# Kernel optimization log

Measured on AMD Instinct MI355X. Metric: run time of the kernel, lower is better.

The kernel has to match this reference:

```python
import jax, jax.numpy as jnp
import numpy as np

N_POI = 1_000_000
R = 10_000
D = 128
H = 4
E = 80_000


def setup_inputs() -> dict:
    key = jax.random.key(0)
    ks = jax.random.split(key, 16)
    s = 0.05
    lin = lambda k: jax.random.normal(k, (D, D), jnp.float32) * s
    return {
        "x": jax.random.normal(ks[0], (N_POI, D), jnp.float32),
        "zone": jax.random.randint(ks[1], (N_POI,), 0, R),
        "edge_index": jax.random.randint(ks[2], (2, E), 0, R),
        "num_regions": R,
        "S": jax.random.normal(ks[3], (D,), jnp.float32) * s,  # PMA seed (num_seeds=1)
        "Wq": lin(ks[4]), "bq": jnp.zeros((D,), jnp.float32),
        "Wk": lin(ks[5]), "bk": jnp.zeros((D,), jnp.float32),
        "Wv": lin(ks[6]), "bv": jnp.zeros((D,), jnp.float32),
        "Wo": lin(ks[7]), "bo": jnp.zeros((D,), jnp.float32),
        "Wg": lin(ks[8]), "bg": jnp.zeros((D,), jnp.float32),  # GCNConv weight/bias
        "prelu_w": jnp.full((D,), 0.25, jnp.float32),
    }


def reference(x, zone, edge_index, num_regions, S, Wq, bq, Wk, bk, Wv, bv, Wo, bo, Wg, bg, prelu_w):
    d = x.shape[1]
    dh = d // H
    # --- PMA over each region (segment attention; seed query shared across regions) ---
    q = (S @ Wq + bq).reshape(H, dh)                     # [H, dh]
    k = (x @ Wk + bk).reshape(-1, H, dh)                 # [N, H, dh]
    v = (x @ Wv + bv).reshape(-1, H, dh)                 # [N, H, dh]
    scores = jnp.einsum('nhd,hd->nh', k, q) / jnp.sqrt(jnp.float32(d))  # Set-Transformer scales by sqrt(dim_V)
    smax = jax.ops.segment_max(scores, zone, num_segments=num_regions)  # [R, H]
    smax = jnp.where(jnp.isfinite(smax), smax, 0.0)
    p = jnp.exp(scores - smax[zone])                     # [N, H]
    denom = jax.ops.segment_sum(p, zone, num_segments=num_regions)      # [R, H]
    wv = jax.ops.segment_sum(p[:, :, None] * v, zone, num_segments=num_regions)  # [R, H, dh]
    attn = wv / jnp.maximum(denom, 1e-9)[:, :, None]
    O = (q[None, :, :] + attn).reshape(num_regions, d)   # residual: Q_ + A @ V_
    O = O + jax.nn.relu(O @ Wo + bo)                     # O + relu(fc_o(O))
    # --- GCNConv (symmetric norm, self loops) ---
    row, col = edge_index[0], edge_index[1]
    sl = jnp.arange(num_regions, dtype=row.dtype)
    row = jnp.concatenate([row, sl])
    col = jnp.concatenate([col, sl])
    deg = jax.ops.segment_sum(jnp.ones_like(col, jnp.float32), col, num_segments=num_regions)
    dinv = jnp.where(deg > 0, 1.0 / jnp.sqrt(deg), 0.0)
    norm = dinv[row] * dinv[col]                         # [E + R]
    h = O @ Wg                                           # [R, D]
    agg = jax.ops.segment_sum(norm[:, None] * h[row], col, num_segments=num_regions)
    out = agg + bg
    # --- PReLU ---
    return jnp.where(out >= 0, out, prelu_w[None, :] * out)
```

## Files before the change

### kernel.cpp

```cpp
#include <hip/hip_runtime.h>
#include <math.h>

__global__ __launch_bounds__(256) void k_init(
    int* __restrict__ izero, int n4, int zb,
    const float* __restrict__ S, const float* __restrict__ Wq, const float* __restrict__ bq,
    const float* __restrict__ Wk, const float* __restrict__ bk,
    float* __restrict__ qvec, float* __restrict__ A, float* __restrict__ cvec) {
  if (blockIdx.x < (unsigned)zb) {
    int i = blockIdx.x * blockDim.x + threadIdx.x;
    if (i < n4) reinterpret_cast<int4*>(izero)[i] = make_int4(0, 0, 0, 0);
    return;
  }
  __shared__ float s_S[128];
  __shared__ float s_q[128];
  const int j = threadIdx.x;
  if (j < 128) s_S[j] = S[j];
  __syncthreads();
  if (j < 128) {
    float acc = bq[j];
    for (int i = 0; i < 128; ++i) acc += s_S[i] * Wq[i * 128 + j];
    qvec[j] = acc;
    s_q[j] = acc;
  }
  __syncthreads();
  if (j < 128) {
    const float scale = 0.088388347648318447f;
    for (int h = 0; h < 4; ++h) {
      float a = 0.f;
      for (int d = 0; d < 32; ++d) a += Wk[j * 128 + h * 32 + d] * s_q[h * 32 + d];
      A[j * 4 + h] = a * scale;
    }
    if (j < 4) {
      float cc = 0.f;
      for (int d = 0; d < 32; ++d) cc += bk[j * 32 + d] * s_q[j * 32 + d];
      cvec[j] = cc * scale;
    }
  }
}

__global__ __launch_bounds__(256) void k_hist2(const int* __restrict__ zone, int N,
                                               const int* __restrict__ ecol, int E,
                                               int* __restrict__ counts, int* __restrict__ ecounts) {
  int i = blockIdx.x * blockDim.x + threadIdx.x;
  if (i < N) {
    atomicAdd(&counts[zone[i]], 1);
  } else if (i < N + E) {
    atomicAdd(&ecounts[ecol[i - N]], 1);
  }
}

__global__ __launch_bounds__(256) void k_scan2(const int* __restrict__ counts, const int* __restrict__ ecounts,
                                               int R, int* __restrict__ startb, int* __restrict__ estartb,
                                               float* __restrict__ dinv) {
  __shared__ int part[256];
  const int t = threadIdx.x;
  const bool edges = (blockIdx.x == 1);
  const int* __restrict__ cnt = edges ? ecounts : counts;
  int* __restrict__ outp = edges ? estartb : startb;
  int chunk = (R + 255) / 256;
  int b = t * chunk, e = min(b + chunk, R);
  int s = 0;
  for (int i = b; i < e; ++i) s += cnt[i];
  part[t] = s;
  __syncthreads();
  for (int off = 1; off < 256; off <<= 1) {
    int v = (t >= off) ? part[t - off] : 0;
    __syncthreads();
    part[t] += v;
    __syncthreads();
  }
  int run = part[t] - s;
  for (int i = b; i < e; ++i) {
    outp[i] = run;
    int c = cnt[i];
    run += c;
    if (edges) dinv[i] = rsqrtf((float)(c + 1));
  }
  if (t == 255) outp[R] = part[255];
}

__global__ __launch_bounds__(256) void k_scatter2(
    const int* __restrict__ zone, int N,
    const int* __restrict__ erow, const int* __restrict__ ecol, int E,
    const int* __restrict__ startb, int* __restrict__ cursor, int* __restrict__ perm,
    const int* __restrict__ estartb, int* __restrict__ ecursor, int* __restrict__ erow_s) {
  int i = blockIdx.x * blockDim.x + threadIdx.x;
  if (i < N) {
    int r = zone[i];
    perm[startb[r] + atomicAdd(&cursor[r], 1)] = i;
  } else if (i < N + E) {
    int e = i - N;
    int c = ecol[e];
    erow_s[estartb[c] + atomicAdd(&ecursor[c], 1)] = erow[e];
  }
}

__global__ __launch_bounds__(256) void k_fused(
    const float* __restrict__ x, const int* __restrict__ perm, const int* __restrict__ startb,
    const float* __restrict__ Aw, const float* __restrict__ cvec,
    float* __restrict__ Xagg, float* __restrict__ denom, int R) {
  const int tid = threadIdx.x;
  const int lane = tid & 63;
  const int half = lane >> 5;
  const int sl = lane & 31;
  const int d0 = sl * 4;
  const int myh = lane & 3;
  const int gw = blockIdx.x * 4 + (tid >> 6);
  const int nw = gridDim.x * 4;

  float a[4][4];
#pragma unroll
  for (int dd = 0; dd < 4; ++dd)
#pragma unroll
    for (int h = 0; h < 4; ++h) a[dd][h] = Aw[(d0 + dd) * 4 + h];
  const float cl = cvec[myh];

  for (int r = gw; r < R; r += nw) {
    const int s0 = startb[r], s1 = startb[r + 1];
    float xagg[4][4] = {};
    float dsum[4] = {};

    int base = s0 + half * 8;
    int idx[8];
#pragma unroll
    for (int k = 0; k < 8; ++k) {
      const int j = base + k;
      idx[k] = (j < s1) ? perm[j] : -1;
    }
    for (; base < s1; base += 16) {
      float4 xv[8];
#pragma unroll
      for (int k = 0; k < 8; ++k) {
        xv[k] = (idx[k] >= 0)
              ? *reinterpret_cast<const float4*>(x + (size_t)idx[k] * 128 + d0)
              : make_float4(0.f, 0.f, 0.f, 0.f);
      }
      int idxn[8];
      const int nb = base + 16;
#pragma unroll
      for (int k = 0; k < 8; ++k) {
        const int j = nb + k;
        idxn[k] = (j < s1) ? perm[j] : -1;
      }
      float red[8];
#pragma unroll
      for (int k = 0; k < 8; ++k) {
        const float4 v = xv[k];
        const float p0 = v.x * a[0][0] + v.y * a[1][0] + v.z * a[2][0] + v.w * a[3][0];
        const float p1 = v.x * a[0][1] + v.y * a[1][1] + v.z * a[2][1] + v.w * a[3][1];
        const float p2 = v.x * a[0][2] + v.y * a[1][2] + v.z * a[2][2] + v.w * a[3][2];
        const float p3 = v.x * a[0][3] + v.y * a[1][3] + v.z * a[2][3] + v.w * a[3][3];
        float a01 = (lane & 1) ? p1 : p0;
        float b01 = (lane & 1) ? p0 : p1;
        a01 += __shfl_xor(b01, 1, 64);
        float a23 = (lane & 1) ? p3 : p2;
        float b23 = (lane & 1) ? p2 : p3;
        a23 += __shfl_xor(b23, 1, 64);
        float aa = (lane & 2) ? a23 : a01;
        float bb = (lane & 2) ? a01 : a23;
        aa += __shfl_xor(bb, 2, 64);
        aa += __shfl_xor(aa, 4, 64);
        aa += __shfl_xor(aa, 8, 64);
        aa += __shfl_xor(aa, 16, 64);
        red[k] = aa;
      }
#pragma unroll
      for (int k = 0; k < 8; ++k) {
        const float e0 = (idx[k] >= 0) ? __expf(red[k] + cl) : 0.f;
        const float e1 = __shfl_xor(e0, 1, 64);
        const float e2 = __shfl_xor(e0, 2, 64);
        const float e3 = __shfl_xor(e0, 3, 64);
        dsum[0] += e0; dsum[1] += e1; dsum[2] += e2; dsum[3] += e3;
        const float4 v = xv[k];
        xagg[0][0] += e0 * v.x; xagg[0][1] += e1 * v.x; xagg[0][2] += e2 * v.x; xagg[0][3] += e3 * v.x;
        xagg[1][0] += e0 * v.y; xagg[1][1] += e1 * v.y; xagg[1][2] += e2 * v.y; xagg[1][3] += e3 * v.y;
        xagg[2][0] += e0 * v.z; xagg[2][1] += e1 * v.z; xagg[2][2] += e2 * v.z; xagg[2][3] += e3 * v.z;
        xagg[3][0] += e0 * v.w; xagg[3][1] += e1 * v.w; xagg[3][2] += e2 * v.w; xagg[3][3] += e3 * v.w;
      }
#pragma unroll
      for (int k = 0; k < 8; ++k) idx[k] = idxn[k];
    }

#pragma unroll
    for (int dd = 0; dd < 4; ++dd)
#pragma unroll
      for (int h = 0; h < 4; ++h) xagg[dd][h] += __shfl_xor(xagg[dd][h], 32, 64);
#pragma unroll
    for (int h = 0; h < 4; ++h) dsum[h] += __shfl_xor(dsum[h], 32, 64);

    if (half == 0) {
      const bool m1 = (myh & 1) != 0;
      const bool m2 = (myh & 2) != 0;
      float outv[4][4];
#pragma unroll
      for (int dd = 0; dd < 4; ++dd) {
        const float b0 = m1 ? xagg[dd][1] : xagg[dd][0];
        const float b1 = m1 ? xagg[dd][0] : xagg[dd][1];
        const float b2 = m1 ? xagg[dd][3] : xagg[dd][2];
        const float b3 = m1 ? xagg[dd][2] : xagg[dd][3];
        outv[0][dd] = m2 ? b2 : b0;
        outv[1][dd] = m2 ? b3 : b1;
        outv[2][dd] = m2 ? b0 : b2;
        outv[3][dd] = m2 ? b1 : b3;
      }
#pragma unroll
      for (int h = 0; h < 4; ++h) {
        const float4 v = make_float4(outv[h][0], outv[h][1], outv[h][2], outv[h][3]);
        *reinterpret_cast<float4*>(Xagg + (size_t)r * 512 + h * 128 + d0) = v;
      }
      if (sl == 0) {
        *reinterpret_cast<float4*>(denom + (size_t)r * 4) =
            make_float4(dsum[0], dsum[1], dsum[2], dsum[3]);
      }
    }
  }
}

__global__ __launch_bounds__(256) void k_epilogue(
    const float* __restrict__ Xagg, const float* __restrict__ denom, const float* __restrict__ qvec,
    const float* __restrict__ Wv, const float* __restrict__ bv,
    const float* __restrict__ Wo, const float* __restrict__ bo,
    const float* __restrict__ Wg, float* __restrict__ hout, int R) {
  const int r0 = blockIdx.x * 8;
  const int tid = threadIdx.x;
  __shared__ float s_xa[8 * 512];
  __shared__ float s_den[8 * 4];
  __shared__ float s_O[8 * 128];
  __shared__ float s_O2[8 * 128];

  for (int t = tid; t < 8 * 512; t += 256) {
    int rl = t >> 9;
    s_xa[t] = (r0 + rl < R) ? Xagg[(size_t)r0 * 512 + t] : 0.f;
  }
  if (tid < 32) {
    int rl = tid >> 2;
    s_den[tid] = (r0 + rl < R) ? denom[r0 * 4 + tid] : 1.f;
  }
  __syncthreads();

  for (int o = tid; o < 1024; o += 256) {
    int rl = o >> 7, t = o & 127, h = t >> 5;
    float acc = 0.f;
    const float* xa = &s_xa[rl * 512 + h * 128];
    for (int j = 0; j < 128; j += 4) {
      float4 x4 = *reinterpret_cast<const float4*>(xa + j);
      acc += x4.x * Wv[j * 128 + t] + x4.y * Wv[(j + 1) * 128 + t]
           + x4.z * Wv[(j + 2) * 128 + t] + x4.w * Wv[(j + 3) * 128 + t];
    }
    float dn = s_den[rl * 4 + h];
    float attn = (acc + dn * bv[t]) / fmaxf(dn, 1e-9f);
    s_O[o] = qvec[t] + attn;
  }
  __syncthreads();

  for (int o = tid; o < 1024; o += 256) {
    int rl = o >> 7, t = o & 127;
    float acc = bo[t];
    const float* ov = &s_O[rl * 128];
    for (int j = 0; j < 128; j += 4) {
      float4 x4 = *reinterpret_cast<const float4*>(ov + j);
      acc += x4.x * Wo[j * 128 + t] + x4.y * Wo[(j + 1) * 128 + t]
           + x4.z * Wo[(j + 2) * 128 + t] + x4.w * Wo[(j + 3) * 128 + t];
    }
    s_O2[o] = s_O[o] + fmaxf(acc, 0.f);
  }
  __syncthreads();

  for (int o = tid; o < 1024; o += 256) {
    int rl = o >> 7, t = o & 127;
    float acc = 0.f;
    const float* ov = &s_O2[rl * 128];
    for (int j = 0; j < 128; j += 4) {
      float4 x4 = *reinterpret_cast<const float4*>(ov + j);
      acc += x4.x * Wg[j * 128 + t] + x4.y * Wg[(j + 1) * 128 + t]
           + x4.z * Wg[(j + 2) * 128 + t] + x4.w * Wg[(j + 3) * 128 + t];
    }
    if (r0 + rl < R) hout[(size_t)(r0 + rl) * 128 + t] = acc;
  }
}

__global__ __launch_bounds__(256) void k_gcn(
    const int* __restrict__ estartb, const int* __restrict__ erow_s,
    const float* __restrict__ dinv, const float* __restrict__ hbuf,
    const float* __restrict__ bg, const float* __restrict__ pw,
    float* __restrict__ out, int R) {
  const int r = blockIdx.x * 4 + (threadIdx.x >> 6);
  if (r >= R) return;
  const int lane = threadIdx.x & 63;
  const int d0 = lane * 2;
  const float dr = dinv[r];
  const float2 hc = *reinterpret_cast<const float2*>(hbuf + (size_t)r * 128 + d0);
  float accx = dr * dr * hc.x;
  float accy = dr * dr * hc.y;
  const int e0 = estartb[r], e1 = estartb[r + 1];
  for (int e = e0; e < e1; ++e) {
    const int rr = erow_s[e];
    const float w = dinv[rr] * dr;
    const float2 hv = *reinterpret_cast<const float2*>(hbuf + (size_t)rr * 128 + d0);
    accx += w * hv.x;
    accy += w * hv.y;
  }
  const float2 b = *reinterpret_cast<const float2*>(bg + d0);
  const float2 pv = *reinterpret_cast<const float2*>(pw + d0);
  const float t0 = accx + b.x;
  const float t1 = accy + b.y;
  out[(size_t)r * 128 + d0]     = (t0 >= 0.f) ? t0 : pv.x * t0;
  out[(size_t)r * 128 + d0 + 1] = (t1 >= 0.f) ? t1 : pv.y * t1;
}

extern "C" void kernel_launch(void* const* d_in, const int* in_sizes, int n_in,
                              void* d_out, int out_size, void* d_ws, size_t ws_size,
                              hipStream_t stream) {
  const float* x   = (const float*)d_in[0];
  const int*   zone = (const int*)d_in[1];
  const int*   eidx = (const int*)d_in[2];
  const float* S   = (const float*)d_in[4];
  const float* Wq  = (const float*)d_in[5];
  const float* bq  = (const float*)d_in[6];
  const float* Wk  = (const float*)d_in[7];
  const float* bk  = (const float*)d_in[8];
  const float* Wv  = (const float*)d_in[9];
  const float* bv  = (const float*)d_in[10];
  const float* Wo  = (const float*)d_in[11];
  const float* bo  = (const float*)d_in[12];
  const float* Wg  = (const float*)d_in[13];
  const float* bg  = (const float*)d_in[14];
  const float* pw  = (const float*)d_in[15];
  float* out = (float*)d_out;

  const int N = in_sizes[0] / 128;
  const int E = in_sizes[2] / 2;
  const int R = out_size / 128;
  const int* erow = eidx;
  const int* ecol = eidx + E;

  char* wsb = (char*)d_ws;
  size_t off = 0;
  auto alloc = [&](size_t bytes) -> void* {
    void* p = wsb + off;
    off = (off + bytes + 255) & ~(size_t)255;
    return p;
  };
  int* izero  = (int*)alloc((size_t)4 * R * 4);
  int* counts = izero;
  int* cursor = izero + R;
  int* ecounts= izero + 2 * R;
  int* ecursor= izero + 3 * R;

  float* qvec  = (float*)alloc(128 * 4);
  float* A     = (float*)alloc(512 * 4);
  float* cvec  = (float*)alloc(4 * 4);
  int*   startb = (int*)alloc((size_t)(R + 1) * 4);
  int*   estartb= (int*)alloc((size_t)(R + 1) * 4);
  float* dinv  = (float*)alloc((size_t)R * 4);
  int*   erow_s= (int*)alloc((size_t)E * 4);
  int*   perm  = (int*)alloc((size_t)N * 4);
  float* Xagg  = (float*)alloc((size_t)R * 512 * 4);
  float* denom = (float*)alloc((size_t)R * 4 * 4);
  float* hbuf  = (float*)alloc((size_t)R * 128 * 4);

  const int n4 = R;
  const int zb = (n4 + 255) / 256;
  k_init<<<zb + 1, 256, 0, stream>>>(izero, n4, zb, S, Wq, bq, Wk, bk, qvec, A, cvec);
  k_hist2<<<(N + E + 255) / 256, 256, 0, stream>>>(zone, N, ecol, E, counts, ecounts);
  k_scan2<<<2, 256, 0, stream>>>(counts, ecounts, R, startb, estartb, dinv);
  k_scatter2<<<(N + E + 255) / 256, 256, 0, stream>>>(zone, N, erow, ecol, E,
                                                      startb, cursor, perm, estartb, ecursor, erow_s);
  k_fused<<<1024, 256, 0, stream>>>(x, perm, startb, A, cvec, Xagg, denom, R);
  k_epilogue<<<(R + 7) / 8, 256, 0, stream>>>(Xagg, denom, qvec, Wv, bv, Wo, bo, Wg, hbuf, R);
  k_gcn<<<(R + 3) / 4, 256, 0, stream>>>(estartb, erow_s, dinv, hbuf, bg, pw, out, R);
}
```

Measured before the change: 371.4 us.

## Record atomic slot positions in histogram and dynamically schedule regions per wave

The histogram pass now stores each element's atomic slot index, so the scatter pass no longer repeats atomics on a second cursor array and only reads the stored position. The q/A precompute moves from the zeroing kernel into a third block of the scan kernel. The fused attention kernel replaces its static grid-stride region assignment with a global atomic work counter, so each wave fetches its next region dynamically to balance uneven region sizes. In exchange this adds 4 MB of position buffers to write and read, plus one atomic per region.

```diff
diff --git a/kernel.cpp b/kernel.cpp
--- a/kernel.cpp
+++ b/kernel.cpp
@@ -1,59 +1,59 @@
 #include <hip/hip_runtime.h>
 #include <math.h>
 
-__global__ __launch_bounds__(256) void k_init(
-    int* __restrict__ izero, int n4, int zb,
+__global__ __launch_bounds__(256) void k_zero(int* __restrict__ p, int n4) {
+  int i = blockIdx.x * blockDim.x + threadIdx.x;
+  if (i < n4) reinterpret_cast<int4*>(p)[i] = make_int4(0, 0, 0, 0);
+}
+
+__global__ __launch_bounds__(256) void k_hist2(const int* __restrict__ zone, int N,
+                                               const int* __restrict__ ecol, int E,
+                                               int* __restrict__ counts, int* __restrict__ ecounts,
+                                               int* __restrict__ pos, int* __restrict__ epos) {
+  int i = blockIdx.x * blockDim.x + threadIdx.x;
+  if (i < N) {
+    pos[i] = atomicAdd(&counts[zone[i]], 1);
+  } else if (i < N + E) {
+    int e = i - N;
+    epos[e] = atomicAdd(&ecounts[ecol[e]], 1);
+  }
+}
+
+__global__ __launch_bounds__(256) void k_scan3(
+    const int* __restrict__ counts, const int* __restrict__ ecounts,
+    int R, int* __restrict__ startb, int* __restrict__ estartb, float* __restrict__ dinv,
     const float* __restrict__ S, const float* __restrict__ Wq, const float* __restrict__ bq,
     const float* __restrict__ Wk, const float* __restrict__ bk,
     float* __restrict__ qvec, float* __restrict__ A, float* __restrict__ cvec) {
-  if (blockIdx.x < (unsigned)zb) {
-    int i = blockIdx.x * blockDim.x + threadIdx.x;
-    if (i < n4) reinterpret_cast<int4*>(izero)[i] = make_int4(0, 0, 0, 0);
+  const int t = threadIdx.x;
+  if (blockIdx.x == 2) {
+    __shared__ float s_S[128];
+    __shared__ float s_q[128];
+    if (t < 128) s_S[t] = S[t];
+    __syncthreads();
+    if (t < 128) {
+      float acc = bq[t];
+      for (int i = 0; i < 128; ++i) acc += s_S[i] * Wq[i * 128 + t];
+      qvec[t] = acc;
+      s_q[t] = acc;
+    }
+    __syncthreads();
+    if (t < 128) {
+      const float scale = 0.088388347648318447f;
+      for (int h = 0; h < 4; ++h) {
+        float a = 0.f;
+        for (int d = 0; d < 32; ++d) a += Wk[t * 128 + h * 32 + d] * s_q[h * 32 + d];
+        A[t * 4 + h] = a * scale;
+      }
+      if (t < 4) {
+        float cc = 0.f;
+        for (int d = 0; d < 32; ++d) cc += bk[t * 32 + d] * s_q[t * 32 + d];
+        cvec[t] = cc * scale;
+      }
+    }
     return;
   }
-  __shared__ float s_S[128];
-  __shared__ float s_q[128];
-  const int j = threadIdx.x;
-  if (j < 128) s_S[j] = S[j];
-  __syncthreads();
-  if (j < 128) {
-    float acc = bq[j];
-    for (int i = 0; i < 128; ++i) acc += s_S[i] * Wq[i * 128 + j];
-    qvec[j] = acc;
-    s_q[j] = acc;
-  }
-  __syncthreads();
-  if (j < 128) {
-    const float scale = 0.088388347648318447f;
-    for (int h = 0; h < 4; ++h) {
-      float a = 0.f;
-      for (int d = 0; d < 32; ++d) a += Wk[j * 128 + h * 32 + d] * s_q[h * 32 + d];
-      A[j * 4 + h] = a * scale;
-    }
-    if (j < 4) {
-      float cc = 0.f;
-      for (int d = 0; d < 32; ++d) cc += bk[j * 32 + d] * s_q[j * 32 + d];
-      cvec[j] = cc * scale;
-    }
-  }
-}
-
-__global__ __launch_bounds__(256) void k_hist2(const int* __restrict__ zone, int N,
-                                               const int* __restrict__ ecol, int E,
-                                               int* __restrict__ counts, int* __restrict__ ecounts) {
-  int i = blockIdx.x * blockDim.x + threadIdx.x;
-  if (i < N) {
-    atomicAdd(&counts[zone[i]], 1);
-  } else if (i < N + E) {
-    atomicAdd(&ecounts[ecol[i - N]], 1);
-  }
-}
-
-__global__ __launch_bounds__(256) void k_scan2(const int* __restrict__ counts, const int* __restrict__ ecounts,
-                                               int R, int* __restrict__ startb, int* __restrict__ estartb,
-                                               float* __restrict__ dinv) {
   __shared__ int part[256];
-  const int t = threadIdx.x;
   const bool edges = (blockIdx.x == 1);
   const int* __restrict__ cnt = edges ? ecounts : counts;
   int* __restrict__ outp = edges ? estartb : startb;
@@ -80,33 +80,29 @@
 }
 
 __global__ __launch_bounds__(256) void k_scatter2(
-    const int* __restrict__ zone, int N,
-    const int* __restrict__ erow, const int* __restrict__ ecol, int E,
-    const int* __restrict__ startb, int* __restrict__ cursor, int* __restrict__ perm,
-    const int* __restrict__ estartb, int* __restrict__ ecursor, int* __restrict__ erow_s) {
+    const int* __restrict__ zone, int N, const int* __restrict__ pos,
+    const int* __restrict__ erow, const int* __restrict__ ecol, int E, const int* __restrict__ epos,
+    const int* __restrict__ startb, int* __restrict__ perm,
+    const int* __restrict__ estartb, int* __restrict__ erow_s) {
   int i = blockIdx.x * blockDim.x + threadIdx.x;
   if (i < N) {
-    int r = zone[i];
-    perm[startb[r] + atomicAdd(&cursor[r], 1)] = i;
+    perm[startb[zone[i]] + pos[i]] = i;
   } else if (i < N + E) {
     int e = i - N;
-    int c = ecol[e];
-    erow_s[estartb[c] + atomicAdd(&ecursor[c], 1)] = erow[e];
+    erow_s[estartb[ecol[e]] + epos[e]] = erow[e];
   }
 }
 
 __global__ __launch_bounds__(256) void k_fused(
     const float* __restrict__ x, const int* __restrict__ perm, const int* __restrict__ startb,
     const float* __restrict__ Aw, const float* __restrict__ cvec,
-    float* __restrict__ Xagg, float* __restrict__ denom, int R) {
+    float* __restrict__ Xagg, float* __restrict__ denom, int R, int* __restrict__ wctr) {
   const int tid = threadIdx.x;
   const int lane = tid & 63;
   const int half = lane >> 5;
   const int sl = lane & 31;
   const int d0 = sl * 4;
   const int myh = lane & 3;
-  const int gw = blockIdx.x * 4 + (tid >> 6);
-  const int nw = gridDim.x * 4;
 
   float a[4][4];
 #pragma unroll
@@ -115,7 +111,11 @@
     for (int h = 0; h < 4; ++h) a[dd][h] = Aw[(d0 + dd) * 4 + h];
   const float cl = cvec[myh];
 
-  for (int r = gw; r < R; r += nw) {
+  int r;
+  if (lane == 0) r = atomicAdd(wctr, 1);
+  r = __shfl(r, 0, 64);
+
+  while (r < R) {
     const int s0 = startb[r], s1 = startb[r + 1];
     float xagg[4][4] = {};
     float dsum[4] = {};
@@ -213,6 +213,9 @@
             make_float4(dsum[0], dsum[1], dsum[2], dsum[3]);
       }
     }
+
+    if (lane == 0) r = atomicAdd(wctr, 1);
+    r = __shfl(r, 0, 64);
   }
 }
 
@@ -341,11 +344,11 @@
     off = (off + bytes + 255) & ~(size_t)255;
     return p;
   };
-  int* izero  = (int*)alloc((size_t)4 * R * 4);
+  const int nz_ints = 2 * R + 4;
+  int* izero  = (int*)alloc((size_t)nz_ints * 4);
   int* counts = izero;
-  int* cursor = izero + R;
-  int* ecounts= izero + 2 * R;
-  int* ecursor= izero + 3 * R;
+  int* ecounts= izero + R;
+  int* wctr   = izero + 2 * R;
 
   float* qvec  = (float*)alloc(128 * 4);
   float* A     = (float*)alloc(512 * 4);
@@ -354,19 +357,21 @@
   int*   estartb= (int*)alloc((size_t)(R + 1) * 4);
   float* dinv  = (float*)alloc((size_t)R * 4);
   int*   erow_s= (int*)alloc((size_t)E * 4);
+  int*   epos  = (int*)alloc((size_t)E * 4);
   int*   perm  = (int*)alloc((size_t)N * 4);
+  int*   pos   = (int*)alloc((size_t)N * 4);
   float* Xagg  = (float*)alloc((size_t)R * 512 * 4);
   float* denom = (float*)alloc((size_t)R * 4 * 4);
   float* hbuf  = (float*)alloc((size_t)R * 128 * 4);
 
-  const int n4 = R;
-  const int zb = (n4 + 255) / 256;
-  k_init<<<zb + 1, 256, 0, stream>>>(izero, n4, zb, S, Wq, bq, Wk, bk, qvec, A, cvec);
-  k_hist2<<<(N + E + 255) / 256, 256, 0, stream>>>(zone, N, ecol, E, counts, ecounts);
-  k_scan2<<<2, 256, 0, stream>>>(counts, ecounts, R, startb, estartb, dinv);
-  k_scatter2<<<(N + E + 255) / 256, 256, 0, stream>>>(zone, N, erow, ecol, E,
-                                                      startb, cursor, perm, estartb, ecursor, erow_s);
-  k_fused<<<1024, 256, 0, stream>>>(x, perm, startb, A, cvec, Xagg, denom, R);
+  const int n4 = (nz_ints + 3) / 4;
+  k_zero<<<(n4 + 255) / 256, 256, 0, stream>>>(izero, n4);
+  k_hist2<<<(N + E + 255) / 256, 256, 0, stream>>>(zone, N, ecol, E, counts, ecounts, pos, epos);
+  k_scan3<<<3, 256, 0, stream>>>(counts, ecounts, R, startb, estartb, dinv,
+                                 S, Wq, bq, Wk, bk, qvec, A, cvec);
+  k_scatter2<<<(N + E + 255) / 256, 256, 0, stream>>>(zone, N, pos, erow, ecol, E, epos,
+                                                      startb, perm, estartb, erow_s);
+  k_fused<<<1024, 256, 0, stream>>>(x, perm, startb, A, cvec, Xagg, denom, R, wctr);
   k_epilogue<<<(R + 7) / 8, 256, 0, stream>>>(Xagg, denom, qvec, Wv, bv, Wo, bo, Wg, hbuf, R);
   k_gcn<<<(R + 3) / 4, 256, 0, stream>>>(estartb, erow_s, dinv, hbuf, bg, pw, out, R);
 }
```

After: 393.2 us. 5.9% more time.

## Stage epilogue weight matrices through shared memory and move q/A setup into scan kernel

Applied to the files above, without the earlier changes.

The epilogue's three 128x128 matvec stages now load the weight matrices in 32-row tiles into shared memory and keep four register accumulators per thread, instead of every thread reading Wv/Wo/Wg straight from global memory. The query/key-projection setup (qvec, A, cvec) moves from the zeroing kernel into a third block of the scan kernel, which makes the zero kernel trivial and hides the serial setup behind the scans. This adds 16 KB of shared memory per block and more barriers, which may reduce occupancy in the epilogue.

```diff
diff --git a/kernel.cpp b/kernel.cpp
--- a/kernel.cpp
+++ b/kernel.cpp
@@ -1,41 +1,9 @@
 #include <hip/hip_runtime.h>
 #include <math.h>
 
-__global__ __launch_bounds__(256) void k_init(
-    int* __restrict__ izero, int n4, int zb,
-    const float* __restrict__ S, const float* __restrict__ Wq, const float* __restrict__ bq,
-    const float* __restrict__ Wk, const float* __restrict__ bk,
-    float* __restrict__ qvec, float* __restrict__ A, float* __restrict__ cvec) {
-  if (blockIdx.x < (unsigned)zb) {
-    int i = blockIdx.x * blockDim.x + threadIdx.x;
-    if (i < n4) reinterpret_cast<int4*>(izero)[i] = make_int4(0, 0, 0, 0);
-    return;
-  }
-  __shared__ float s_S[128];
-  __shared__ float s_q[128];
-  const int j = threadIdx.x;
-  if (j < 128) s_S[j] = S[j];
-  __syncthreads();
-  if (j < 128) {
-    float acc = bq[j];
-    for (int i = 0; i < 128; ++i) acc += s_S[i] * Wq[i * 128 + j];
-    qvec[j] = acc;
-    s_q[j] = acc;
-  }
-  __syncthreads();
-  if (j < 128) {
-    const float scale = 0.088388347648318447f;
-    for (int h = 0; h < 4; ++h) {
-      float a = 0.f;
-      for (int d = 0; d < 32; ++d) a += Wk[j * 128 + h * 32 + d] * s_q[h * 32 + d];
-      A[j * 4 + h] = a * scale;
-    }
-    if (j < 4) {
-      float cc = 0.f;
-      for (int d = 0; d < 32; ++d) cc += bk[j * 32 + d] * s_q[j * 32 + d];
-      cvec[j] = cc * scale;
-    }
-  }
+__global__ __launch_bounds__(256) void k_zero(int* __restrict__ p, int n4) {
+  int i = blockIdx.x * blockDim.x + threadIdx.x;
+  if (i < n4) reinterpret_cast<int4*>(p)[i] = make_int4(0, 0, 0, 0);
 }
 
 __global__ __launch_bounds__(256) void k_hist2(const int* __restrict__ zone, int N,
@@ -49,11 +17,41 @@
   }
 }
 
-__global__ __launch_bounds__(256) void k_scan2(const int* __restrict__ counts, const int* __restrict__ ecounts,
-                                               int R, int* __restrict__ startb, int* __restrict__ estartb,
-                                               float* __restrict__ dinv) {
+__global__ __launch_bounds__(256) void k_scan3(
+    const int* __restrict__ counts, const int* __restrict__ ecounts,
+    int R, int* __restrict__ startb, int* __restrict__ estartb, float* __restrict__ dinv,
+    const float* __restrict__ S, const float* __restrict__ Wq, const float* __restrict__ bq,
+    const float* __restrict__ Wk, const float* __restrict__ bk,
+    float* __restrict__ qvec, float* __restrict__ A, float* __restrict__ cvec) {
+  const int t = threadIdx.x;
+  if (blockIdx.x == 2) {
+    __shared__ float s_S[128];
+    __shared__ float s_q[128];
+    if (t < 128) s_S[t] = S[t];
+    __syncthreads();
+    if (t < 128) {
+      float acc = bq[t];
+      for (int i = 0; i < 128; ++i) acc += s_S[i] * Wq[i * 128 + t];
+      qvec[t] = acc;
+      s_q[t] = acc;
+    }
+    __syncthreads();
+    if (t < 128) {
+      const float scale = 0.088388347648318447f;
+      for (int h = 0; h < 4; ++h) {
+        float a = 0.f;
+        for (int d = 0; d < 32; ++d) a += Wk[t * 128 + h * 32 + d] * s_q[h * 32 + d];
+        A[t * 4 + h] = a * scale;
+      }
+      if (t < 4) {
+        float cc = 0.f;
+        for (int d = 0; d < 32; ++d) cc += bk[t * 32 + d] * s_q[t * 32 + d];
+        cvec[t] = cc * scale;
+      }
+    }
+    return;
+  }
   __shared__ int part[256];
-  const int t = threadIdx.x;
   const bool edges = (blockIdx.x == 1);
   const int* __restrict__ cnt = edges ? ecounts : counts;
   int* __restrict__ outp = edges ? estartb : startb;
@@ -227,6 +225,7 @@
   __shared__ float s_den[8 * 4];
   __shared__ float s_O[8 * 128];
   __shared__ float s_O2[8 * 128];
+  __shared__ float s_W[32 * 128];
 
   for (int t = tid; t < 8 * 512; t += 256) {
     int rl = t >> 9;
@@ -238,44 +237,80 @@
   }
   __syncthreads();
 
-  for (int o = tid; o < 1024; o += 256) {
-    int rl = o >> 7, t = o & 127, h = t >> 5;
-    float acc = 0.f;
-    const float* xa = &s_xa[rl * 512 + h * 128];
-    for (int j = 0; j < 128; j += 4) {
-      float4 x4 = *reinterpret_cast<const float4*>(xa + j);
-      acc += x4.x * Wv[j * 128 + t] + x4.y * Wv[(j + 1) * 128 + t]
-           + x4.z * Wv[(j + 2) * 128 + t] + x4.w * Wv[(j + 3) * 128 + t];
-    }
-    float dn = s_den[rl * 4 + h];
-    float attn = (acc + dn * bv[t]) / fmaxf(dn, 1e-9f);
+  float acc[4] = {0.f, 0.f, 0.f, 0.f};
+  for (int jb = 0; jb < 128; jb += 32) {
+    for (int w = tid * 4; w < 32 * 128; w += 1024)
+      *reinterpret_cast<float4*>(&s_W[w]) = *reinterpret_cast<const float4*>(&Wv[jb * 128 + w]);
+    __syncthreads();
+#pragma unroll
+    for (int k = 0; k < 4; ++k) {
+      const int o = tid + k * 256;
+      const int rl = o >> 7, t = o & 127, h = (t >> 5);
+      const float* xa = &s_xa[rl * 512 + h * 128 + jb];
+      float a = acc[k];
+#pragma unroll 8
+      for (int j = 0; j < 32; ++j) a += xa[j] * s_W[j * 128 + t];
+      acc[k] = a;
+    }
+    __syncthreads();
+  }
+#pragma unroll
+  for (int k = 0; k < 4; ++k) {
+    const int o = tid + k * 256;
+    const int rl = o >> 7, t = o & 127, h = (t >> 5);
+    const float dn = s_den[rl * 4 + h];
+    const float attn = (acc[k] + dn * bv[t]) / fmaxf(dn, 1e-9f);
     s_O[o] = qvec[t] + attn;
+    acc[k] = 0.f;
   }
   __syncthreads();
 
-  for (int o = tid; o < 1024; o += 256) {
-    int rl = o >> 7, t = o & 127;
-    float acc = bo[t];
-    const float* ov = &s_O[rl * 128];
-    for (int j = 0; j < 128; j += 4) {
-      float4 x4 = *reinterpret_cast<const float4*>(ov + j);
-      acc += x4.x * Wo[j * 128 + t] + x4.y * Wo[(j + 1) * 128 + t]
-           + x4.z * Wo[(j + 2) * 128 + t] + x4.w * Wo[(j + 3) * 128 + t];
-    }
-    s_O2[o] = s_O[o] + fmaxf(acc, 0.f);
+  for (int jb = 0; jb < 128; jb += 32) {
+    for (int w = tid * 4; w < 32 * 128; w += 1024)
+      *reinterpret_cast<float4*>(&s_W[w]) = *reinterpret_cast<const float4*>(&Wo[jb * 128 + w]);
+    __syncthreads();
+#pragma unroll
+    for (int k = 0; k < 4; ++k) {
+      const int o = tid + k * 256;
+      const int rl = o >> 7, t = o & 127;
+      const float* ov = &s_O[rl * 128 + jb];
+      float a = acc[k];
+#pragma unroll 8
+      for (int j = 0; j < 32; ++j) a += ov[j] * s_W[j * 128 + t];
+      acc[k] = a;
+    }
+    __syncthreads();
+  }
+#pragma unroll
+  for (int k = 0; k < 4; ++k) {
+    const int o = tid + k * 256;
+    const int t = o & 127;
+    s_O2[o] = s_O[o] + fmaxf(acc[k] + bo[t], 0.f);
+    acc[k] = 0.f;
   }
   __syncthreads();
 
-  for (int o = tid; o < 1024; o += 256) {
-    int rl = o >> 7, t = o & 127;
-    float acc = 0.f;
-    const float* ov = &s_O2[rl * 128];
-    for (int j = 0; j < 128; j += 4) {
-      float4 x4 = *reinterpret_cast<const float4*>(ov + j);
-      acc += x4.x * Wg[j * 128 + t] + x4.y * Wg[(j + 1) * 128 + t]
-           + x4.z * Wg[(j + 2) * 128 + t] + x4.w * Wg[(j + 3) * 128 + t];
-    }
-    if (r0 + rl < R) hout[(size_t)(r0 + rl) * 128 + t] = acc;
+  for (int jb = 0; jb < 128; jb += 32) {
+    for (int w = tid * 4; w < 32 * 128; w += 1024)
+      *reinterpret_cast<float4*>(&s_W[w]) = *reinterpret_cast<const float4*>(&Wg[jb * 128 + w]);
+    __syncthreads();
+#pragma unroll
+    for (int k = 0; k < 4; ++k) {
+      const int o = tid + k * 256;
+      const int rl = o >> 7, t = o & 127;
+      const float* ov = &s_O2[rl * 128 + jb];
+      float a = acc[k];
+#pragma unroll 8
+      for (int j = 0; j < 32; ++j) a += ov[j] * s_W[j * 128 + t];
+      acc[k] = a;
+    }
+    __syncthreads();
+  }
+#pragma unroll
+  for (int k = 0; k < 4; ++k) {
+    const int o = tid + k * 256;
+    const int rl = o >> 7, t = o & 127;
+    if (r0 + rl < R) hout[(size_t)(r0 + rl) * 128 + t] = acc[k];
   }
 }
 
@@ -360,10 +395,10 @@
   float* hbuf  = (float*)alloc((size_t)R * 128 * 4);
 
   const int n4 = R;
-  const int zb = (n4 + 255) / 256;
-  k_init<<<zb + 1, 256, 0, stream>>>(izero, n4, zb, S, Wq, bq, Wk, bk, qvec, A, cvec);
+  k_zero<<<(n4 + 255) / 256, 256, 0, stream>>>(izero, n4);
   k_hist2<<<(N + E + 255) / 256, 256, 0, stream>>>(zone, N, ecol, E, counts, ecounts);
-  k_scan2<<<2, 256, 0, stream>>>(counts, ecounts, R, startb, estartb, dinv);
+  k_scan3<<<3, 256, 0, stream>>>(counts, ecounts, R, startb, estartb, dinv,
+                                 S, Wq, bq, Wk, bk, qvec, A, cvec);
   k_scatter2<<<(N + E + 255) / 256, 256, 0, stream>>>(zone, N, erow, ecol, E,
                                                       startb, cursor, perm, estartb, ecursor, erow_s);
   k_fused<<<1024, 256, 0, stream>>>(x, perm, startb, A, cvec, Xagg, denom, R);
```

Measured after the change: 377.8 us. About the same (+1.7%).
